# Optimization experiments

Measured on AMD Instinct MI355X. Metric: run time of the kernel, lower is better.

## Reference

```python
import jax, jax.numpy as jnp
import numpy as np

# dims
B, C, N, T = 8, 64, 500, 12      # batch, channels (c_in=c_out=nhid), nodes, time
H, F = 4, 64                      # nheads, nhid per head
GDEP = 2
ALPHA = 0.05                      # mixprop residual mix
LEAK = 0.2                        # leakyrelu slope in attention


def setup_inputs() -> dict:
    key = jax.random.key(0)
    ks = jax.random.split(key, 9)
    x = jax.random.normal(ks[0], (B, C, N, T), jnp.float32)
    adj = (jax.random.uniform(ks[1], (N, N)) < 0.05).astype(jnp.float32)
    # per-head GAT params stacked on head axis
    W = jax.random.normal(ks[2], (H, C, F), jnp.float32) * 0.05   # head projection
    a1 = jax.random.normal(ks[3], (H, F), jnp.float32) * 0.05     # a[:F]
    a2 = jax.random.normal(ks[4], (H, F), jnp.float32) * 0.05     # a[F:]
    # GAT output mlp: Conv2d 1x1, (H*F) -> F
    Wg = jax.random.normal(ks[5], (F, H * F), jnp.float32) * 0.05
    bg = jnp.zeros((F,), jnp.float32)
    # mixprop mlp: (GDEP+1)*C -> C
    Wm = jax.random.normal(ks[6], (C, (GDEP + 1) * C), jnp.float32) * 0.05
    bm = jnp.zeros((C,), jnp.float32)
    return {"x": x, "adj": adj, "W": W, "a1": a1, "a2": a2,
            "Wg": Wg, "bg": bg, "Wm": Wm, "bm": bm}


def _gat(h, mask, W, a1, a2, Wg, bg):
    # h: [B,C,N,T]; eval mode (dropout = identity)
    hp = jnp.transpose(h, (0, 3, 2, 1))                 # [B,T,N,C]
    Wh = jnp.einsum('btnc,hcf->bhtnf', hp, W)           # [B,H,T,N,F]
    e1 = jnp.einsum('bhtnf,hf->bhtn', Wh, a1)           # src term
    e2 = jnp.einsum('bhtnf,hf->bhtn', Wh, a2)           # dst term
    e = jax.nn.leaky_relu(e1[..., :, None] + e2[..., None, :], LEAK)  # [B,H,T,N,N]
    e = jnp.where(mask, e, jnp.float32(-9e15))
    att = jax.nn.softmax(e, axis=-1)
    hpr = jax.nn.elu(jnp.einsum('bhtnm,bhtmf->bhtnf', att, Wh))       # [B,H,T,N,F]
    # concat heads along channel dim -> [B, H*F, N, T]
    cat = jnp.transpose(hpr, (0, 1, 4, 3, 2)).reshape(B, H * F, N, T)
    # 1x1 conv mix
    return jnp.einsum('bcnt,oc->bont', cat, Wg) + bg[None, :, None, None]


def reference(x, adj, W, a1, a2, Wg, bg, Wm, bm):
    mask = (adj + jnp.eye(N, dtype=adj.dtype)) > 0      # self-loops added
    h = x
    outs = [h]
    for _ in range(GDEP):
        h = ALPHA * x + (1.0 - ALPHA) * _gat(h, mask, W, a1, a2, Wg, bg)
        outs.append(h)
    ho = jnp.concatenate(outs, axis=1)                  # [B,(GDEP+1)*C,N,T]
    return jnp.einsum('bcnt,oc->bont', ho, Wm) + bm[None, :, None, None]
```

## Files before the change

kernel.cpp:

```cpp
#include <hip/hip_runtime.h>
#include <hip/hip_bf16.h>
#include <math.h>

#define BB 8
#define CC 64
#define NN 500
#define TT 12
#define HH 4
#define FF 64
#define CT (CC*TT)
#define HF (HH*FF)
#define NBT (HH*TT)
#define NBHT (BB*NBT)
#define NROWS (BB*HH*TT*NN)
#define NNODE (BB*NN)
#define BSR 200
#define KST 68
#define WTS 520
#define WTILE 32768

typedef unsigned short ushort_t;
typedef unsigned int uint_t;
typedef __attribute__((ext_vector_type(8))) short short8;
typedef __attribute__((ext_vector_type(4))) float floatx4;

static __device__ __forceinline__ ushort_t f2bf(float v) {
    __hip_bfloat16 h = __float2bfloat16(v);
    ushort_t u;
    __builtin_memcpy(&u, &h, 2);
    return u;
}

static __device__ __forceinline__ float bf2f(ushort_t u) {
    return __uint_as_float(((uint_t)u) << 16);
}

static __device__ __forceinline__ uint_t pkbf(float a, float b) {
    __hip_bfloat162 h = __float22bfloat162_rn(make_float2(a, b));
    uint_t u;
    __builtin_memcpy(&u, &h, 4);
    return u;
}


__global__ __launch_bounds__(256) void k016_setup(const float* __restrict__ adj,
                                                  const float* __restrict__ W,
                                                  const float* __restrict__ a1,
                                                  const float* __restrict__ a2,
                                                  const float* __restrict__ Wm,
                                                  const float* __restrict__ Wg,
                                                  const float* __restrict__ x,
                                                  uint_t* __restrict__ maskbits,
                                                  ushort_t* __restrict__ pAB,
                                                  ushort_t* __restrict__ WmB,
                                                  ushort_t* __restrict__ WgB,
                                                  ushort_t* __restrict__ WtB,
                                                  ushort_t* __restrict__ xB,
                                                  ushort_t* __restrict__ WhT) {
    __shared__ float tile[16*776];
    int blk = blockIdx.x;
    if (blk < 32) {
        int idx = blk * 256 + threadIdx.x;
        int n = idx >> 4, j = idx & 15;
        uint_t v = 0;
        if (n < NN) {
            int m0 = j * 32;
            for (int i = 0; i < 32; ++i) {
                int m = m0 + i;
                bool p = (m < NN) && (adj[n*NN + m] > 0.f || m == n);
                v |= (p ? 1u : 0u) << i;
            }
        }
        maskbits[idx] = v;
        return;
    }
    if (blk < 225) {
        int idx = (blk - 32) * 256 + threadIdx.x;
        if (idx < HH*16*CC) {
            int h   = idx >> 10;
            int rem = idx & 1023;
            int row = rem >> 6, c = rem & 63;
            ushort_t val = 0;
            if (row < 4) {
                const float* av = (row < 2) ? a1 : a2;
                float s = 0.f;
                for (int f = 0; f < FF; ++f)
                    s += W[(h*CC + c)*FF + f] * av[h*FF + f];
                if ((row & 1) == 0) val = f2bf(s);
                else                val = f2bf(s - bf2f(f2bf(s)));
            }
            pAB[idx] = val;
        }
        int j = idx - HH*16*CC;
        if (j >= 0 && j < CC*3*CC) {
            WmB[j] = f2bf(Wm[j]);
        }
        int j2 = idx - (HH*16*CC + CC*3*CC);
        if (j2 >= 0 && j2 < FF*HF) {
            WgB[j2] = f2bf(Wg[j2]);
        }
        int j3 = idx - (HH*16*CC + CC*3*CC + FF*HF);
        if (j3 >= 0 && j3 < HH*CC*FF) {
            int h = j3 >> 12, rem = j3 & 4095;
            int f = rem >> 6, c = rem & 63;
            WtB[j3] = f2bf(W[h*4096 + c*64 + f]);
        }
        return;
    }
    if (blk >= 481) {
        int task = (blk - 481) * 256 + threadIdx.x;
        int tilei = task >> 6;
        int ft    = (task >> 4) & 3;
        int r     = task & 15;
        ushort_t* base = WhT + (size_t)tilei*WTILE + (size_t)(15*4 + ft)*512;
        *(uint_t*)(base + 2*128 + r*8 + 4) = 0;
        *(uint_t*)(base + 2*128 + r*8 + 6) = 0;
        *(short8*)(base + 3*128 + r*8) = (short8){0,0,0,0,0,0,0,0};
        return;
    }
    int xblk = blk - 225;
    int b  = xblk >> 5;
    int n0 = (xblk & 31) * 16;
    for (int idx = threadIdx.x; idx < CC*16*TT; idx += 256) {
        int c   = idx / (16*TT);
        int rem = idx % (16*TT);
        int nl  = rem / TT;
        int t   = rem % TT;
        int n   = n0 + nl;
        if (n < NN)
            tile[nl*776 + c*TT + t] = x[((b*CC + c)*NN + n)*TT + t];
    }
    __syncthreads();
    for (int idx = threadIdx.x; idx < 16*384; idx += 256) {
        int nl = idx / 384, j = idx % 384;
        int t = j >> 5, c2 = j & 31;
        int n = n0 + nl;
        if (n < NN) {
            float v0 = tile[nl*776 + (2*c2)*TT + t];
            float v1 = tile[nl*776 + (2*c2 + 1)*TT + t];
            *(uint_t*)&xB[(size_t)(b*NN + n)*CT + t*64 + 2*c2] = pkbf(v0, v1);
        }
    }
}

__global__ __launch_bounds__(256) void k2_wh_e(const ushort_t* __restrict__ hinB,
                                               const ushort_t* __restrict__ WtB,
                                               const ushort_t* __restrict__ pAB,
                                               ushort_t* __restrict__ WhT,
                                               float* __restrict__ e1,
                                               float* __restrict__ e2) {
    __shared__ ushort_t WTu[4*TT*WTS];
    __shared__ ushort_t Bs[8][TT*KST];
    int tid  = threadIdx.x;
    int wid  = tid >> 6;
    int lane = tid & 63;
    int quad = lane >> 4;
    int r    = lane & 15;
    int b    = blockIdx.x / 63;
    int nl0  = (blockIdx.x % 63) * 8;

    for (int i = tid; i < 8*TT*8; i += 256) {
        int u = i / 96, rem = i % 96;
        int t = rem >> 3, c8 = rem & 7;
        int node = b*NN + nl0 + u;
        if (node > NNODE-1) node = NNODE-1;
        short8 v = *(const short8*)(hinB + (size_t)node*CT + t*64 + c8*8);
        *(short8*)&Bs[u][t*KST + c8*8] = v;
    }
    __syncthreads();

    ushort_t* WTl = WTu + wid*(TT*WTS);

    short8 Afr[4][2];
    #pragma unroll
    for (int mt = 0; mt < 4; ++mt)
        #pragma unroll
        for (int kc = 0; kc < 2; ++kc)
            Afr[mt][kc] = *(const short8*)(WtB + wid*4096 +
                                           (mt*16 + r)*64 + kc*32 + quad*8);
    short8 pfr[2];
    #pragma unroll
    for (int kc = 0; kc < 2; ++kc)
        pfr[kc] = *(const short8*)(pAB + wid*1024 + r*64 + kc*32 + quad*8);

    int rcl = r < TT ? r : TT-1;

    for (int u = 0; u < 8; ++u) {
        bool valid = (nl0 + u) < NN;
        floatx4 C[4];
        floatx4 C5 = (floatx4){0.f,0.f,0.f,0.f};
        #pragma unroll
        for (int mt = 0; mt < 4; ++mt) C[mt] = (floatx4){0.f,0.f,0.f,0.f};
        #pragma unroll
        for (int kc = 0; kc < 2; ++kc) {
            short8 bfr = *(const short8*)&Bs[u][rcl*KST + kc*32 + quad*8];
            #pragma unroll
            for (int mt = 0; mt < 4; ++mt)
                C[mt] = __builtin_amdgcn_mfma_f32_16x16x32_bf16(Afr[mt][kc], bfr, C[mt], 0, 0, 0);
            C5 = __builtin_amdgcn_mfma_f32_16x16x32_bf16(pfr[kc], bfr, C5, 0, 0, 0);
        }
        if (quad == 0 && r < TT && valid) {
            int ebase = ((b*HH + wid)*TT + r)*NN + nl0 + u;
            e1[ebase] = C5[0] + C5[1];
            e2[ebase] = C5[2] + C5[3];
        }
        if (r < TT) {
            #pragma unroll
            for (int mt = 0; mt < 4; ++mt) {
                #pragma unroll
                for (int reg = 0; reg < 4; ++reg) {
                    int f = mt*16 + quad*4 + reg;
                    WTl[r*WTS + f*8 + u] = valid ? f2bf(C[mt][reg]) : (ushort_t)0;
                }
            }
        }
    }

    {
        int ki = nl0 >> 5;
        int q  = (nl0 >> 3) & 3;
        int ft = lane >> 4, rr = lane & 15;
        size_t tbase = (size_t)(b*NBT + wid*TT) * WTILE
                     + (size_t)(ki*4 + ft)*512 + q*128 + rr*8;
        #pragma unroll
        for (int t = 0; t < TT; ++t) {
            short8 v = *(const short8*)&WTl[t*WTS + lane*8];
            *(short8*)(WhT + tbase + (size_t)t*WTILE) = v;
        }
    }
}

__global__ __launch_bounds__(256) void k42_fused(const ushort_t* __restrict__ hprB,
                                                 const ushort_t* __restrict__ WgB,
                                                 const float* __restrict__ bg,
                                                 const ushort_t* __restrict__ xB,
                                                 ushort_t* __restrict__ h1B,
                                                 const ushort_t* __restrict__ WtB,
                                                 const ushort_t* __restrict__ pAB,
                                                 ushort_t* __restrict__ WhT,
                                                 float* __restrict__ e1,
                                                 float* __restrict__ e2) {
    __shared__ ushort_t WTu[4*TT*WTS];
    __shared__ ushort_t Bs[8][TT*KST];
    int tid  = threadIdx.x;
    int wid  = tid >> 6;
    int lane = tid & 63;
    int quad = lane >> 4;
    int r    = lane & 15;
    int b    = blockIdx.x / 63;
    int nl0  = (blockIdx.x % 63) * 8;

    for (int i = tid; i < 8*TT*8; i += 256) {
        int u = i / 96, rem = i % 96;
        int t = rem >> 3, c8 = rem & 7;
        int node = b*NN + nl0 + u;
        if (node > NNODE-1) node = NNODE-1;
        *(short8*)&Bs[u][t*KST + c8*8] =
            *(const short8*)(xB + (size_t)node*CT + t*64 + c8*8);
    }
    __syncthreads();

    {
        short8 Ag[4][8];
        #pragma unroll
        for (int ot = 0; ot < 4; ++ot)
            #pragma unroll
            for (int kc = 0; kc < 8; ++kc)
                Ag[ot][kc] = *(const short8*)(WgB + (size_t)(ot*16 + r)*HF + kc*32 + quad*8);
        float4 bgv[4];
        #pragma unroll
        for (int ot = 0; ot < 4; ++ot)
            bgv[ot] = *(const float4*)(bg + ot*16 + quad*4);

        int tcl = r < TT ? r : TT-1;

        for (int p = 0; p < 2; ++p) {
            int u  = wid + p*4;
            int nl = nl0 + u;
            int node = b*NN + nl;
            int nodec = node > NNODE-1 ? NNODE-1 : node;
            const ushort_t* P = hprB + (size_t)nodec * (NBT*FF);

            floatx4 C[4];
            #pragma unroll
            for (int ot = 0; ot < 4; ++ot) C[ot] = (floatx4){0.f,0.f,0.f,0.f};
            #pragma unroll
            for (int kc = 0; kc < 8; ++kc) {
                int k = kc*32 + quad*8;
                int h = k >> 6, f0 = k & 63;
                short8 bfr = *(const short8*)(P + (h*TT + tcl)*FF + f0);
                #pragma unroll
                for (int ot = 0; ot < 4; ++ot)
                    C[ot] = __builtin_amdgcn_mfma_f32_16x16x32_bf16(Ag[ot][kc], bfr, C[ot], 0, 0, 0);
            }

            if (r < TT && nl < NN) {
                ushort_t* hp = h1B + (size_t)node*CT;
                #pragma unroll
                for (int ot = 0; ot < 4; ++ot) {
                    #pragma unroll
                    for (int rp = 0; rp < 4; rp += 2) {
                        int o = ot*16 + quad*4 + rp;
                        uint_t xu = *(const uint_t*)&Bs[u][r*KST + o];
                        float x0 = bf2f((ushort_t)(xu & 0xffffu));
                        float x1 = bf2f((ushort_t)(xu >> 16));
                        float v0 = C[ot][rp]   + bgv[ot][rp];
                        float v1 = C[ot][rp+1] + bgv[ot][rp+1];
                        uint_t pv = pkbf(0.05f*x0 + 0.95f*v0,
                                         0.05f*x1 + 0.95f*v1);
                        *(uint_t*)&Bs[u][r*KST + o] = pv;
                        *(uint_t*)&hp[r*64 + o]     = pv;
                    }
                }
            }
        }
    }
    __syncthreads();

    ushort_t* WTl = WTu + wid*(TT*WTS);

    short8 Afr[4][2];
    #pragma unroll
    for (int mt = 0; mt < 4; ++mt)
        #pragma unroll
        for (int kc = 0; kc < 2; ++kc)
            Afr[mt][kc] = *(const short8*)(WtB + wid*4096 +
                                           (mt*16 + r)*64 + kc*32 + quad*8);
    short8 pfr[2];
    #pragma unroll
    for (int kc = 0; kc < 2; ++kc)
        pfr[kc] = *(const short8*)(pAB + wid*1024 + r*64 + kc*32 + quad*8);

    int rcl = r < TT ? r : TT-1;

    for (int u = 0; u < 8; ++u) {
        bool valid = (nl0 + u) < NN;
        floatx4 C[4];
        floatx4 C5 = (floatx4){0.f,0.f,0.f,0.f};
        #pragma unroll
        for (int mt = 0; mt < 4; ++mt) C[mt] = (floatx4){0.f,0.f,0.f,0.f};
        #pragma unroll
        for (int kc = 0; kc < 2; ++kc) {
            short8 bfr = *(const short8*)&Bs[u][rcl*KST + kc*32 + quad*8];
            #pragma unroll
            for (int mt = 0; mt < 4; ++mt)
                C[mt] = __builtin_amdgcn_mfma_f32_16x16x32_bf16(Afr[mt][kc], bfr, C[mt], 0, 0, 0);
            C5 = __builtin_amdgcn_mfma_f32_16x16x32_bf16(pfr[kc], bfr, C5, 0, 0, 0);
        }
        if (quad == 0 && r < TT && valid) {
            int ebase = ((b*HH + wid)*TT + r)*NN + nl0 + u;
            e1[ebase] = C5[0] + C5[1];
            e2[ebase] = C5[2] + C5[3];
        }
        if (r < TT) {
            #pragma unroll
            for (int mt = 0; mt < 4; ++mt) {
                #pragma unroll
                for (int reg = 0; reg < 4; ++reg) {
                    int f = mt*16 + quad*4 + reg;
                    WTl[r*WTS + f*8 + u] = valid ? f2bf(C[mt][reg]) : (ushort_t)0;
                }
            }
        }
    }

    {
        int ki = nl0 >> 5;
        int q  = (nl0 >> 3) & 3;
        int ft = lane >> 4, rr = lane & 15;
        size_t tbase = (size_t)(b*NBT + wid*TT) * WTILE
                     + (size_t)(ki*4 + ft)*512 + q*128 + rr*8;
        #pragma unroll
        for (int t = 0; t < TT; ++t) {
            short8 v = *(const short8*)&WTl[t*WTS + lane*8];
            *(short8*)(WhT + tbase + (size_t)t*WTILE) = v;
        }
    }
}

__global__ __launch_bounds__(256, 3) void k3_attn(const ushort_t* __restrict__ WhT,
                                                  const float* __restrict__ e1,
                                                  const float* __restrict__ e2,
                                                  const uint_t* __restrict__ maskbits,
                                                  ushort_t* __restrict__ hprB) {
    __shared__ float  e2s[512];
    __shared__ uint_t mks[256*17];
    int tid  = threadIdx.x;
    int wid  = tid >> 6;
    int lane = tid & 63;
    int bht  = blockIdx.x >> 1;
    int half = blockIdx.x & 1;
    int b    = bht / NBT;
    int ht   = bht % NBT;

    const float* e1p = e1 + (size_t)bht * NN;
    const float* e2p = e2 + (size_t)bht * NN;
    const ushort_t* WTp = WhT + (size_t)bht * WTILE;
    const float L2E = 1.4426950408889634f;

    {
        int i = tid;
        e2s[i] = (i < NN) ? e2p[i] * L2E : 0.f;
        i = tid + 256;
        e2s[i] = (i < NN) ? e2p[i] * L2E : 0.f;
    }
    for (int i = tid; i < 256*16; i += 256) {
        int rl = i >> 4, dw = i & 15;
        mks[rl*17 + dw] = maskbits[(half*256 + rl)*16 + dw];
    }
    __syncthreads();

    int quad = lane >> 4;
    int r    = lane & 15;

    const short8 ONES = {0x3F80,0x3F80,0x3F80,0x3F80,
                         0x3F80,0x3F80,0x3F80,0x3F80};

    float e1v[4];
    #pragma unroll
    for (int u = 0; u < 4; ++u) {
        int nrow = half*256 + (wid*4 + u)*16 + r;
        e1v[u] = ((nrow < NN) ? e1p[nrow] : 0.f) * L2E;
    }
    int rl0 = wid*64 + r;

    const ushort_t* WTl8 = WTp + lane*8;

    floatx4 C[4][4];
    floatx4 Cs[4];
    #pragma unroll
    for (int u = 0; u < 4; ++u) {
        Cs[u] = (floatx4){0.f,0.f,0.f,0.f};
        #pragma unroll
        for (int ft = 0; ft < 4; ++ft) C[u][ft] = (floatx4){0.f,0.f,0.f,0.f};
    }

    short8 nbf[4];
    #pragma unroll
    for (int ft = 0; ft < 4; ++ft)
        nbf[ft] = *(const short8*)(WTl8 + (size_t)ft*512);

    #pragma unroll
    for (int ki = 0; ki < 16; ++ki) {
        int kb = ki*32 + quad*8;

        short8 b0 = nbf[0], b1 = nbf[1], b2 = nbf[2], b3 = nbf[3];
        if (ki < 15) {
            #pragma unroll
            for (int ft = 0; ft < 4; ++ft)
                nbf[ft] = *(const short8*)(WTl8 + (size_t)((ki+1)*4 + ft)*512);
        }

        float4 ea = *(const float4*)&e2s[kb];
        float4 eb = *(const float4*)&e2s[kb + 4];
        float ev[8] = {ea.x,ea.y,ea.z,ea.w, eb.x,eb.y,eb.z,eb.w};

        #pragma unroll
        for (int u = 0; u < 4; ++u) {
            uint_t md    = mks[(rl0 + u*16)*17 + ki];
            uint_t mbits = md >> (quad*8);
            union { uint_t w[4]; short8 s; } av;
            #pragma unroll
            for (int p = 0; p < 4; ++p) {
                float s0 = e1v[u] + ev[2*p];
                float s1 = e1v[u] + ev[2*p+1];
                float g0 = fmaxf(s0, 0.2f*s0);
                float g1 = fmaxf(s1, 0.2f*s1);
                float x0 = __builtin_amdgcn_exp2f(g0);
                float x1 = __builtin_amdgcn_exp2f(g1);
                x0 = (mbits & (1u << (2*p)))     ? x0 : 0.f;
                x1 = (mbits & (1u << (2*p + 1))) ? x1 : 0.f;
                av.w[p] = pkbf(x0, x1);
            }
            __builtin_amdgcn_s_setprio(1);
            C[u][0] = __builtin_amdgcn_mfma_f32_16x16x32_bf16(av.s, b0, C[u][0], 0, 0, 0);
            C[u][1] = __builtin_amdgcn_mfma_f32_16x16x32_bf16(av.s, b1, C[u][1], 0, 0, 0);
            C[u][2] = __builtin_amdgcn_mfma_f32_16x16x32_bf16(av.s, b2, C[u][2], 0, 0, 0);
            C[u][3] = __builtin_amdgcn_mfma_f32_16x16x32_bf16(av.s, b3, C[u][3], 0, 0, 0);
            Cs[u]   = __builtin_amdgcn_mfma_f32_16x16x32_bf16(av.s, ONES, Cs[u], 0, 0, 0);
            __builtin_amdgcn_s_setprio(0);
        }
    }

    #pragma unroll
    for (int u = 0; u < 4; ++u) {
        int n0 = half*256 + (wid*4 + u)*16;
        #pragma unroll
        for (int reg = 0; reg < 4; ++reg) {
            int n = n0 + quad*4 + reg;
            if (n < NN) {
                float inv = 1.0f / Cs[u][reg];
                size_t base = ((size_t)(b*NN + n)*NBT + ht)*FF;
                #pragma unroll
                for (int ft = 0; ft < 4; ++ft) {
                    float v = C[u][ft][reg] * inv;
                    v = v > 0.f ? v : __expf(v) - 1.f;
                    hprB[base + ft*16 + r] = f2bf(v);
                }
            }
        }
    }
}

__global__ __launch_bounds__(256) void k45_fused(const ushort_t* __restrict__ hprB,
                                                 const ushort_t* __restrict__ WgB,
                                                 const float* __restrict__ bg,
                                                 const ushort_t* __restrict__ xB,
                                                 const ushort_t* __restrict__ h1B,
                                                 const ushort_t* __restrict__ WmB,
                                                 const float* __restrict__ bm,
                                                 float* __restrict__ out) {
    __shared__ ushort_t Bs[4][TT*BSR];
    __shared__ float    So[4][CT];
    int wid  = threadIdx.x >> 6;
    int lane = threadIdx.x & 63;
    int quad = lane >> 4;
    int r    = lane & 15;

    int node = blockIdx.x*4 + wid;
    ushort_t* Bw = Bs[wid];

    {
        const ushort_t* xp = xB  + (size_t)node*CT;
        const ushort_t* hp = h1B + (size_t)node*CT;
        for (int task = lane; task < 96; task += 64) {
            int t = task >> 3, c8 = task & 7;
            *(short8*)&Bw[t*BSR + c8*8]      = *(const short8*)(xp + t*64 + c8*8);
            *(short8*)&Bw[t*BSR + 64 + c8*8] = *(const short8*)(hp + t*64 + c8*8);
        }
    }

    {
        short8 Afr[4][8];
        #pragma unroll
        for (int ot = 0; ot < 4; ++ot)
            #pragma unroll
            for (int kc = 0; kc < 8; ++kc)
                Afr[ot][kc] = *(const short8*)(WgB + (size_t)(ot*16 + r)*HF + kc*32 + quad*8);
        float4 bgv[4];
        #pragma unroll
        for (int ot = 0; ot < 4; ++ot)
            bgv[ot] = *(const float4*)(bg + ot*16 + quad*4);

        int tcl = r < TT ? r : TT-1;
        const ushort_t* P = hprB + (size_t)node * (NBT*FF);

        floatx4 C[4];
        #pragma unroll
        for (int ot = 0; ot < 4; ++ot) C[ot] = (floatx4){0.f,0.f,0.f,0.f};
        #pragma unroll
        for (int kc = 0; kc < 8; ++kc) {
            int k = kc*32 + quad*8;
            int h = k >> 6, f0 = k & 63;
            short8 bfr = *(const short8*)(P + (h*TT + tcl)*FF + f0);
            #pragma unroll
            for (int ot = 0; ot < 4; ++ot)
                C[ot] = __builtin_amdgcn_mfma_f32_16x16x32_bf16(Afr[ot][kc], bfr, C[ot], 0, 0, 0);
        }

        if (r < TT) {
            #pragma unroll
            for (int ot = 0; ot < 4; ++ot) {
                #pragma unroll
                for (int rp = 0; rp < 4; rp += 2) {
                    int o = ot*16 + quad*4 + rp;
                    float v0 = C[ot][rp]   + bgv[ot][rp];
                    float v1 = C[ot][rp+1] + bgv[ot][rp+1];
                    float x0 = bf2f(Bw[r*BSR + o]);
                    float x1 = bf2f(Bw[r*BSR + o + 1]);
                    float h20 = 0.05f*x0 + 0.95f*v0;
                    float h21 = 0.05f*x1 + 0.95f*v1;
                    *(uint_t*)&Bw[r*BSR + 128 + o] = pkbf(h20, h21);
                }
            }
        }
    }

    {
        short8 Am[4][6];
        #pragma unroll
        for (int ot = 0; ot < 4; ++ot)
            #pragma unroll
            for (int kc = 0; kc < 6; ++kc)
                Am[ot][kc] = *(const short8*)(WmB + (size_t)(ot*16 + r)*(3*CC) + kc*32 + quad*8);

        int trd = r < TT ? r : TT-1;
        floatx4 C2[4];
        #pragma unroll
        for (int ot = 0; ot < 4; ++ot) C2[ot] = (floatx4){0.f,0.f,0.f,0.f};
        #pragma unroll
        for (int kc = 0; kc < 6; ++kc) {
            short8 bfr = *(const short8*)&Bw[trd*BSR + kc*32 + quad*8];
            #pragma unroll
            for (int ot = 0; ot < 4; ++ot)
                C2[ot] = __builtin_amdgcn_mfma_f32_16x16x32_bf16(Am[ot][kc], bfr, C2[ot], 0, 0, 0);
        }

        if (r < TT) {
            #pragma unroll
            for (int ot = 0; ot < 4; ++ot) {
                float4 bmv = *(const float4*)(bm + ot*16 + quad*4);
                #pragma unroll
                for (int reg = 0; reg < 4; ++reg) {
                    int o = ot*16 + quad*4 + reg;
                    So[wid][o*TT + r] = C2[ot][reg] + bmv[reg];
                }
            }
        }
    }
    __syncthreads();

    {
        int o = threadIdx.x >> 2;
        int q = threadIdx.x & 3;
        int nodeq = blockIdx.x*4 + q;
        int bq = nodeq / NN, nq = nodeq % NN;
        float* op = out + ((size_t)(bq*CC + o)*NN + nq)*TT;
        const float* Sp = So[q] + o*TT;
        *(float4*)&op[0] = *(const float4*)&Sp[0];
        *(float4*)&op[4] = *(const float4*)&Sp[4];
        *(float4*)&op[8] = *(const float4*)&Sp[8];
    }
}

extern "C" void kernel_launch(void* const* d_in, const int* in_sizes, int n_in,
                              void* d_out, int out_size, void* d_ws, size_t ws_size,
                              hipStream_t stream) {
    const float* x   = (const float*)d_in[0];
    const float* adj = (const float*)d_in[1];
    const float* W   = (const float*)d_in[2];
    const float* a1  = (const float*)d_in[3];
    const float* a2  = (const float*)d_in[4];
    const float* Wg  = (const float*)d_in[5];
    const float* bg  = (const float*)d_in[6];
    const float* Wm  = (const float*)d_in[7];
    const float* bm  = (const float*)d_in[8];
    float* out = (float*)d_out;

    char* ws = (char*)d_ws;
    size_t off = 0;
    auto alloc = [&](size_t bytes) -> void* {
        void* p = ws + off;
        off += (bytes + 255) & ~(size_t)255;
        return p;
    };

    uint_t* maskbits = (uint_t*)alloc((size_t)512 * 16 * 4);
    ushort_t* pAB = (ushort_t*)alloc((size_t)HH*16*CC * 2);
    ushort_t* WmB = (ushort_t*)alloc((size_t)CC*3*CC * 2);
    ushort_t* WgB = (ushort_t*)alloc((size_t)FF*HF * 2);
    ushort_t* WtB = (ushort_t*)alloc((size_t)HH*CC*FF * 2);
    ushort_t* xB  = (ushort_t*)alloc((size_t)NNODE * CT * 2);
    ushort_t* WhT  = (ushort_t*)alloc((size_t)NBHT * WTILE * 2);
    ushort_t* hprB = (ushort_t*)alloc((size_t)NNODE * NBT * FF * 2);
    float* e1   = (float*)alloc((size_t)NROWS * sizeof(float));
    float* e2   = (float*)alloc((size_t)NROWS * sizeof(float));
    ushort_t* h1B = (ushort_t*)alloc((size_t)NNODE * CT * 2);
    (void)ws_size;

    k016_setup<<<577, 256, 0, stream>>>(adj, W, a1, a2, Wm, Wg, x,
                                        maskbits, pAB, WmB, WgB, WtB, xB, WhT);

    k2_wh_e <<<8*63,    256, 0, stream>>>(xB, WtB, pAB, WhT, e1, e2);
    k3_attn <<<NBHT*2,  256, 0, stream>>>(WhT, e1, e2, maskbits, hprB);

    k42_fused<<<8*63,   256, 0, stream>>>(hprB, WgB, bg, xB, h1B,
                                          WtB, pAB, WhT, e1, e2);

    k3_attn <<<NBHT*2,  256, 0, stream>>>(WhT, e1, e2, maskbits, hprB);

    k45_fused<<<NNODE/4, 256, 0, stream>>>(hprB, WgB, bg, xB, h1B, WmB, bm, out);
}
```

Measured before the change: 247.6 us.

## Replace dense MFMA attention with CSR sparse gather attention kernel

Builds a CSR (rowPtr/colIdx) of the ~5% masked adjacency in a new single-block kernel. The dense bf16 MFMA attention over all 500 neighbors is replaced with a per-row scalar loop over only the valid neighbors. The loop factors exp(leaky(e1+e2)) as max(E1*E2, F1*F2) to avoid per-edge exp, and Wh is stored row-major by node so neighbor rows can be gathered as 128-byte vectors. This skips the large amount of masked-out work, but gives up tensor cores, adds irregular gathers and load imbalance, and adds a serial single-thread prefix scan kernel.

```diff
diff --git a/kernel.cpp b/kernel.cpp
--- a/kernel.cpp
+++ b/kernel.cpp
@@ -23,6 +23,7 @@
 typedef unsigned int uint_t;
 typedef __attribute__((ext_vector_type(8))) short short8;
 typedef __attribute__((ext_vector_type(4))) float floatx4;
+typedef __attribute__((ext_vector_type(2))) float float2v;
 
 static __device__ __forceinline__ ushort_t f2bf(float v) {
     __hip_bfloat16 h = __float2bfloat16(v);
@@ -40,6 +41,13 @@
     uint_t u;
     __builtin_memcpy(&u, &h, 4);
     return u;
+}
+
+static __device__ __forceinline__ float2v bf2x2(uint_t u) {
+    float2v r;
+    r.x = __uint_as_float(u << 16);
+    r.y = __uint_as_float(u & 0xffff0000u);
+    return r;
 }
 
 
@@ -55,8 +63,7 @@
                                                   ushort_t* __restrict__ WmB,
                                                   ushort_t* __restrict__ WgB,
                                                   ushort_t* __restrict__ WtB,
-                                                  ushort_t* __restrict__ xB,
-                                                  ushort_t* __restrict__ WhT) {
+                                                  ushort_t* __restrict__ xB) {
     __shared__ float tile[16*776];
     int blk = blockIdx.x;
     if (blk < 32) {
@@ -107,17 +114,6 @@
         }
         return;
     }
-    if (blk >= 481) {
-        int task = (blk - 481) * 256 + threadIdx.x;
-        int tilei = task >> 6;
-        int ft    = (task >> 4) & 3;
-        int r     = task & 15;
-        ushort_t* base = WhT + (size_t)tilei*WTILE + (size_t)(15*4 + ft)*512;
-        *(uint_t*)(base + 2*128 + r*8 + 4) = 0;
-        *(uint_t*)(base + 2*128 + r*8 + 6) = 0;
-        *(short8*)(base + 3*128 + r*8) = (short8){0,0,0,0,0,0,0,0};
-        return;
-    }
     int xblk = blk - 225;
     int b  = xblk >> 5;
     int n0 = (xblk & 31) * 16;
@@ -139,6 +135,38 @@
             float v0 = tile[nl*776 + (2*c2)*TT + t];
             float v1 = tile[nl*776 + (2*c2 + 1)*TT + t];
             *(uint_t*)&xB[(size_t)(b*NN + n)*CT + t*64 + 2*c2] = pkbf(v0, v1);
+        }
+    }
+}
+
+__global__ __launch_bounds__(256) void k0_csr(const uint_t* __restrict__ maskbits,
+                                              uint_t* __restrict__ rowPtr,
+                                              ushort_t* __restrict__ colIdx) {
+    __shared__ uint_t cnt[NN];
+    __shared__ uint_t rp[NN + 1];
+    int tid = threadIdx.x;
+    for (int n = tid; n < NN; n += 256) {
+        uint_t c = 0;
+        for (int d = 0; d < 16; ++d) c += __popc(maskbits[n*16 + d]);
+        cnt[n] = c;
+    }
+    __syncthreads();
+    if (tid == 0) {
+        uint_t s = 0;
+        for (int n = 0; n < NN; ++n) { rp[n] = s; s += cnt[n]; }
+        rp[NN] = s;
+    }
+    __syncthreads();
+    for (int n = tid; n <= NN; n += 256) rowPtr[n] = rp[n];
+    for (int n = tid; n < NN; n += 256) {
+        uint_t p = rp[n];
+        for (int d = 0; d < 16; ++d) {
+            uint_t bits = maskbits[n*16 + d];
+            while (bits) {
+                int i = __ffs(bits) - 1;
+                colIdx[p++] = (ushort_t)(d*32 + i);
+                bits &= bits - 1;
+            }
         }
     }
 }
@@ -217,15 +245,12 @@
     }
 
     {
-        int ki = nl0 >> 5;
-        int q  = (nl0 >> 3) & 3;
-        int ft = lane >> 4, rr = lane & 15;
-        size_t tbase = (size_t)(b*NBT + wid*TT) * WTILE
-                     + (size_t)(ki*4 + ft)*512 + q*128 + rr*8;
-        #pragma unroll
         for (int t = 0; t < TT; ++t) {
-            short8 v = *(const short8*)&WTl[t*WTS + lane*8];
-            *(short8*)(WhT + tbase + (size_t)t*WTILE) = v;
+            ushort_t* wp = WhT + (size_t)(b*NBT + wid*TT + t) * WTILE
+                         + (size_t)nl0*64 + lane;
+            #pragma unroll
+            for (int u = 0; u < 8; ++u)
+                wp[u*64] = WTl[t*WTS + lane*8 + u];
         }
     }
 }
@@ -365,140 +390,82 @@
     }
 
     {
-        int ki = nl0 >> 5;
-        int q  = (nl0 >> 3) & 3;
-        int ft = lane >> 4, rr = lane & 15;
-        size_t tbase = (size_t)(b*NBT + wid*TT) * WTILE
-                     + (size_t)(ki*4 + ft)*512 + q*128 + rr*8;
-        #pragma unroll
         for (int t = 0; t < TT; ++t) {
-            short8 v = *(const short8*)&WTl[t*WTS + lane*8];
-            *(short8*)(WhT + tbase + (size_t)t*WTILE) = v;
-        }
-    }
-}
-
-__global__ __launch_bounds__(256, 3) void k3_attn(const ushort_t* __restrict__ WhT,
-                                                  const float* __restrict__ e1,
-                                                  const float* __restrict__ e2,
-                                                  const uint_t* __restrict__ maskbits,
-                                                  ushort_t* __restrict__ hprB) {
-    __shared__ float  e2s[512];
-    __shared__ uint_t mks[256*17];
+            ushort_t* wp = WhT + (size_t)(b*NBT + wid*TT + t) * WTILE
+                         + (size_t)nl0*64 + lane;
+            #pragma unroll
+            for (int u = 0; u < 8; ++u)
+                wp[u*64] = WTl[t*WTS + lane*8 + u];
+        }
+    }
+}
+
+__global__ __launch_bounds__(256) void k3_sparse(const ushort_t* __restrict__ WhT,
+                                                 const float* __restrict__ e1,
+                                                 const float* __restrict__ e2,
+                                                 const uint_t* __restrict__ rowPtr,
+                                                 const ushort_t* __restrict__ colIdx,
+                                                 ushort_t* __restrict__ hprB) {
+    __shared__ float E2s[NN];
+    __shared__ float F2s[NN];
     int tid  = threadIdx.x;
-    int wid  = tid >> 6;
-    int lane = tid & 63;
     int bht  = blockIdx.x >> 1;
     int half = blockIdx.x & 1;
     int b    = bht / NBT;
     int ht   = bht % NBT;
-
     const float* e1p = e1 + (size_t)bht * NN;
     const float* e2p = e2 + (size_t)bht * NN;
-    const ushort_t* WTp = WhT + (size_t)bht * WTILE;
+    const ushort_t* WT = WhT + (size_t)bht * WTILE;
     const float L2E = 1.4426950408889634f;
 
-    {
-        int i = tid;
-        e2s[i] = (i < NN) ? e2p[i] * L2E : 0.f;
-        i = tid + 256;
-        e2s[i] = (i < NN) ? e2p[i] * L2E : 0.f;
-    }
-    for (int i = tid; i < 256*16; i += 256) {
-        int rl = i >> 4, dw = i & 15;
-        mks[rl*17 + dw] = maskbits[(half*256 + rl)*16 + dw];
-    }
-    __syncthreads();
-
-    int quad = lane >> 4;
-    int r    = lane & 15;
-
-    const short8 ONES = {0x3F80,0x3F80,0x3F80,0x3F80,
-                         0x3F80,0x3F80,0x3F80,0x3F80};
-
-    float e1v[4];
+    for (int i = tid; i < NN; i += 256) {
+        float v = e2p[i] * L2E;
+        E2s[i] = __builtin_amdgcn_exp2f(v);
+        F2s[i] = __builtin_amdgcn_exp2f(0.2f * v);
+    }
+    __syncthreads();
+
+    if (tid >= 250) return;
+    int n = half * 250 + tid;
+
+    float ev = e1p[n] * L2E;
+    float E1 = __builtin_amdgcn_exp2f(ev);
+    float F1 = __builtin_amdgcn_exp2f(0.2f * ev);
+
+    int p0 = (int)rowPtr[n], p1 = (int)rowPtr[n + 1];
+
+    float2v acc[32];
     #pragma unroll
-    for (int u = 0; u < 4; ++u) {
-        int nrow = half*256 + (wid*4 + u)*16 + r;
-        e1v[u] = ((nrow < NN) ? e1p[nrow] : 0.f) * L2E;
-    }
-    int rl0 = wid*64 + r;
-
-    const ushort_t* WTl8 = WTp + lane*8;
-
-    floatx4 C[4][4];
-    floatx4 Cs[4];
+    for (int g = 0; g < 32; ++g) acc[g] = (float2v){0.f, 0.f};
+    float den = 0.f;
+
+    int mNext = (int)colIdx[p0];
+    for (int k = p0; k < p1; ++k) {
+        int m = mNext;
+        mNext = (k + 1 < p1) ? (int)colIdx[k + 1] : 0;
+        float w = fmaxf(E1 * E2s[m], F1 * F2s[m]);
+        den += w;
+        float2v wv = {w, w};
+        const uint_t* col = (const uint_t*)(WT + (size_t)m * 64);
+        #pragma unroll
+        for (int g = 0; g < 8; ++g) {
+            uint4 d = *(const uint4*)(col + g * 4);
+            acc[g*4+0] += wv * bf2x2(d.x);
+            acc[g*4+1] += wv * bf2x2(d.y);
+            acc[g*4+2] += wv * bf2x2(d.z);
+            acc[g*4+3] += wv * bf2x2(d.w);
+        }
+    }
+
+    float inv = 1.f / den;
+    uint_t* op = (uint_t*)(hprB + ((size_t)(b*NN + n)*NBT + ht)*FF);
     #pragma unroll
-    for (int u = 0; u < 4; ++u) {
-        Cs[u] = (floatx4){0.f,0.f,0.f,0.f};
-        #pragma unroll
-        for (int ft = 0; ft < 4; ++ft) C[u][ft] = (floatx4){0.f,0.f,0.f,0.f};
-    }
-
-    short8 nbf[4];
-    #pragma unroll
-    for (int ft = 0; ft < 4; ++ft)
-        nbf[ft] = *(const short8*)(WTl8 + (size_t)ft*512);
-
-    #pragma unroll
-    for (int ki = 0; ki < 16; ++ki) {
-        int kb = ki*32 + quad*8;
-
-        short8 b0 = nbf[0], b1 = nbf[1], b2 = nbf[2], b3 = nbf[3];
-        if (ki < 15) {
-            #pragma unroll
-            for (int ft = 0; ft < 4; ++ft)
-                nbf[ft] = *(const short8*)(WTl8 + (size_t)((ki+1)*4 + ft)*512);
-        }
-
-        float4 ea = *(const float4*)&e2s[kb];
-        float4 eb = *(const float4*)&e2s[kb + 4];
-        float ev[8] = {ea.x,ea.y,ea.z,ea.w, eb.x,eb.y,eb.z,eb.w};
-
-        #pragma unroll
-        for (int u = 0; u < 4; ++u) {
-            uint_t md    = mks[(rl0 + u*16)*17 + ki];
-            uint_t mbits = md >> (quad*8);
-            union { uint_t w[4]; short8 s; } av;
-            #pragma unroll
-            for (int p = 0; p < 4; ++p) {
-                float s0 = e1v[u] + ev[2*p];
-                float s1 = e1v[u] + ev[2*p+1];
-                float g0 = fmaxf(s0, 0.2f*s0);
-                float g1 = fmaxf(s1, 0.2f*s1);
-                float x0 = __builtin_amdgcn_exp2f(g0);
-                float x1 = __builtin_amdgcn_exp2f(g1);
-                x0 = (mbits & (1u << (2*p)))     ? x0 : 0.f;
-                x1 = (mbits & (1u << (2*p + 1))) ? x1 : 0.f;
-                av.w[p] = pkbf(x0, x1);
-            }
-            __builtin_amdgcn_s_setprio(1);
-            C[u][0] = __builtin_amdgcn_mfma_f32_16x16x32_bf16(av.s, b0, C[u][0], 0, 0, 0);
-            C[u][1] = __builtin_amdgcn_mfma_f32_16x16x32_bf16(av.s, b1, C[u][1], 0, 0, 0);
-            C[u][2] = __builtin_amdgcn_mfma_f32_16x16x32_bf16(av.s, b2, C[u][2], 0, 0, 0);
-            C[u][3] = __builtin_amdgcn_mfma_f32_16x16x32_bf16(av.s, b3, C[u][3], 0, 0, 0);
-            Cs[u]   = __builtin_amdgcn_mfma_f32_16x16x32_bf16(av.s, ONES, Cs[u], 0, 0, 0);
-            __builtin_amdgcn_s_setprio(0);
-        }
-    }
-
-    #pragma unroll
-    for (int u = 0; u < 4; ++u) {
-        int n0 = half*256 + (wid*4 + u)*16;
-        #pragma unroll
-        for (int reg = 0; reg < 4; ++reg) {
-            int n = n0 + quad*4 + reg;
-            if (n < NN) {
-                float inv = 1.0f / Cs[u][reg];
-                size_t base = ((size_t)(b*NN + n)*NBT + ht)*FF;
-                #pragma unroll
-                for (int ft = 0; ft < 4; ++ft) {
-                    float v = C[u][ft][reg] * inv;
-                    v = v > 0.f ? v : __expf(v) - 1.f;
-                    hprB[base + ft*16 + r] = f2bf(v);
-                }
-            }
-        }
+    for (int g = 0; g < 32; ++g) {
+        float v0 = acc[g].x * inv;
+        float v1 = acc[g].y * inv;
+        v0 = v0 > 0.f ? v0 : __expf(v0) - 1.f;
+        v1 = v1 > 0.f ? v1 : __expf(v1) - 1.f;
+        op[g] = pkbf(v0, v1);
     }
 }
 
@@ -656,18 +623,21 @@
     float* e1   = (float*)alloc((size_t)NROWS * sizeof(float));
     float* e2   = (float*)alloc((size_t)NROWS * sizeof(float));
     ushort_t* h1B = (ushort_t*)alloc((size_t)NNODE * CT * 2);
+    uint_t* rowPtr = (uint_t*)alloc((size_t)(NN + 1) * 4);
+    ushort_t* colIdx = (ushort_t*)alloc((size_t)NN * 512 * 2);
     (void)ws_size;
 
-    k016_setup<<<577, 256, 0, stream>>>(adj, W, a1, a2, Wm, Wg, x,
-                                        maskbits, pAB, WmB, WgB, WtB, xB, WhT);
+    k016_setup<<<481, 256, 0, stream>>>(adj, W, a1, a2, Wm, Wg, x,
+                                        maskbits, pAB, WmB, WgB, WtB, xB);
+    k0_csr<<<1, 256, 0, stream>>>(maskbits, rowPtr, colIdx);
 
     k2_wh_e <<<8*63,    256, 0, stream>>>(xB, WtB, pAB, WhT, e1, e2);
-    k3_attn <<<NBHT*2,  256, 0, stream>>>(WhT, e1, e2, maskbits, hprB);
+    k3_sparse<<<NBHT*2, 256, 0, stream>>>(WhT, e1, e2, rowPtr, colIdx, hprB);
 
     k42_fused<<<8*63,   256, 0, stream>>>(hprB, WgB, bg, xB, h1B,
                                           WtB, pAB, WhT, e1, e2);
 
-    k3_attn <<<NBHT*2,  256, 0, stream>>>(WhT, e1, e2, maskbits, hprB);
+    k3_sparse<<<NBHT*2, 256, 0, stream>>>(WhT, e1, e2, rowPtr, colIdx, hprB);
 
     k45_fused<<<NNODE/4, 256, 0, stream>>>(hprB, WgB, bg, xB, h1B, WmB, bm, out);
 }
```

Measured after the change: 381.4 us. 54.0% more time.
